# Optimization experiments

Hardware: AMD Instinct MI355X
Metric: run time of the kernel (lower is better)

## Reference

```python
import jax, jax.numpy as jnp
from jax import lax
import numpy as np

NBINS = 50

def _make_filters():
    coords = np.linspace(-1.0, 1.0, 3)
    zz, yy, xx = np.meshgrid(coords, coords, coords, indexing='ij')
    gf = []
    for freq in [2.0, 4.0]:
        for ang in [0.0, np.pi / 4, np.pi / 2, 3 * np.pi / 4]:
            gauss = np.exp(-(xx ** 2 + yy ** 2 + zz ** 2) / 0.5)
            f = gauss * np.cos(freq * (xx * np.cos(ang) + yy * np.sin(ang)))
            f = f - f.mean()
            s = f.std(ddof=1)  # torch std is unbiased
            if s > 1e-8:
                f = f / s
            gf.append(f)
    gf = np.stack(gf)[:, None].astype(np.float32)  # (8,1,3,3,3)
    lf = []
    for axis in range(3):
        for sign in [1, -1]:
            f = np.zeros((3, 3, 3), np.float32)
            f[1, 1, 1] = 1.0
            idx = [1, 1, 1]
            idx[axis] += sign
            f[tuple(idx)] = -1.0
            lf.append(f)
    lf = np.stack(lf)[:, None].astype(np.float32)  # (6,1,3,3,3)
    return gf, lf

def setup_inputs() -> dict:
    key = jax.random.key(0)
    k1, k2 = jax.random.split(key)
    B, D, H, W = 4, 96, 160, 160
    x = jax.random.uniform(k1, (B, 1, D, H, W), jnp.float32, minval=-1.0, maxval=1.0)
    mask = (jax.random.uniform(k2, (B, 1, D, H, W), jnp.float32) > 0.5).astype(jnp.float32)
    gf, lf = _make_filters()
    return {"x": x, "mask": mask, "gabor_filters": jnp.asarray(gf), "lbp_filters": jnp.asarray(lf)}

def _hu_stats(v, mf):
    # v, mf: (B,D,H,W); mf is 0/1 float mask
    n = mf.sum((1, 2, 3))                      # (B,)
    nn = jnp.maximum(n, 1.0)
    mu = (mf * v).sum((1, 2, 3)) / nn
    diff = (v - mu[:, None, None, None]) * mf
    var = (diff ** 2).sum((1, 2, 3)) / jnp.maximum(n - 1.0, 1.0)  # unbiased, like torch .std()
    sigma = jnp.sqrt(var) + 1e-8
    z = diff / sigma[:, None, None, None]
    skew = (z ** 3).sum((1, 2, 3)) / nn
    kurt = (z ** 4).sum((1, 2, 3)) / nn - 3.0
    # histogram over [-1,1] with 50 bins; torch.histc ignores out-of-range, last bin inclusive
    w = mf * ((v >= -1.0) & (v <= 1.0)).astype(v.dtype)
    idx = jnp.clip(jnp.floor((v + 1.0) * (NBINS / 2.0)).astype(jnp.int32), 0, NBINS - 1)
    hist = jax.vmap(lambda i, wb: jnp.zeros((NBINS,), v.dtype).at[i.ravel()].add(wb.ravel()))(idx, w)
    p = hist / (hist.sum(-1, keepdims=True) + 1e-8)
    ent = -(p * jnp.log(p + 1e-8)).sum(-1)
    valid = (n >= 10.0).astype(v.dtype)
    return jnp.stack([mu, sigma, skew, kurt, ent], axis=1) * valid[:, None]  # (B,5)

def _glcm_proxy(v, m):
    # v: (B,D,H,W) float; m: (B,D,H,W) bool
    rows = []
    for axis in range(3):
        a = axis + 1
        sl1 = tuple(slice(None, -1) if i == a else slice(None) for i in range(4))
        sl2 = tuple(slice(1, None) if i == a else slice(None) for i in range(4))
        d = v[sl1] - v[sl2]
        mp = (m[sl1] & m[sl2]).astype(v.dtype)
        s = mp.sum((1, 2, 3))
        ss = jnp.maximum(s, 1.0)
        con = (mp * d * d).sum((1, 2, 3)) / ss
        hom = (mp / (1.0 + d * d)).sum((1, 2, 3)) / ss
        ok = (s >= 4.0).astype(v.dtype)
        rows += [con * ok, hom * ok]
    return jnp.stack(rows, axis=1)  # (B,6)

def _forward(x, mask, gabor_filters, lbp_filters):
    v = x[:, 0]                       # (B,D,H,W)
    m = mask[:, 0] > 0.5              # bool
    mf = m.astype(x.dtype)
    hu = _hu_stats(v, mf)             # (B,5)
    dn = ('NCDHW', 'OIDHW', 'NCDHW')
    pad = [(1, 1)] * 3
    gab = lax.conv_general_dilated(x, gabor_filters, (1, 1, 1), pad, dimension_numbers=dn)
    lung_vol = jnp.clip(mask.sum((2, 3, 4)), 1.0, None)      # (B,1)
    gab_feat = jnp.abs(gab * mask).sum((2, 3, 4)) / lung_vol  # (B,8)
    lbp = lax.conv_general_dilated(x, lbp_filters, (1, 1, 1), pad, dimension_numbers=dn)
    lbp = lbp * mask
    lbp_feat = ((lbp > 0).astype(x.dtype) * mask).sum((2, 3, 4)) / lung_vol  # (B,6)
    glcm = _glcm_proxy(v, m)          # (B,6)
    return jnp.concatenate([hu, gab_feat, lbp_feat, glcm], axis=1)  # (B,25)

def reference(x, mask, gabor_filters, lbp_filters):
    return _forward(x, mask, gabor_filters, lbp_filters)
```

## Files before the change

kernel.cpp:

```cpp
#include <hip/hip_runtime.h>
#include <math.h>

#define B_    4
#define D_    96
#define H_    160
#define W_    160
#define HW_   (H_ * W_)
#define NVOX  (D_ * H_ * W_)
#define NBINS 50
#define NQR   28
#define CPB   256
#define PART_F (B_ * NQR * CPB)
#define HIST_U PART_F
#define WQ_F   (PART_F + 200)
#define LASTP ((D_ - 1) * HW_)

typedef float f2 __attribute__((ext_vector_type(2)));

__device__ __forceinline__ float rfl(float v) {
    return __uint_as_float(__builtin_amdgcn_readfirstlane(__float_as_uint(v)));
}

__global__ __launch_bounds__(64) void radiomics_weights(
    const float* __restrict__ gf, const float* __restrict__ lf,
    float* __restrict__ ws)
{
    const int lane = threadIdx.x;
    __shared__ float sCs[8][5], sR[8], sMO[8], sMC[8];
    if (lane < 8) {
        const int f = lane;
        float O9[9], C9[9];
        float mC = 0.f, mO = 0.f;
#pragma unroll
        for (int k = 0; k < 9; ++k) {
            O9[k] = gf[f * 27 + k];
            C9[k] = gf[f * 27 + 9 + k];
            mC += C9[k]; mO += O9[k];
        }
        mC *= (1.f / 9.f); mO *= (1.f / 9.f);
        float cov = 0.f, var = 0.f;
#pragma unroll
        for (int k = 0; k < 9; ++k) {
            float c = C9[k] - mC, o = O9[k] - mO;
            cov += c * o; var += c * c;
        }
        sR[f] = cov / var; sMO[f] = mO; sMC[f] = mC;
#pragma unroll
        for (int j = 0; j < 4; ++j) sCs[f][j] = 0.5f * (C9[j] + C9[8 - j]);
        sCs[f][4] = C9[4];
    }
    __syncthreads();
    if (lane == 0) {
        float* wq = ws + WQ_F;
        float gz0 = 0.f;
        for (int f = 0; f < 8; ++f) gz0 += sR[f];
        gz0 *= 0.125f;
        wq[0] = gz0;
        float df[8];
        for (int f = 0; f < 8; ++f) df[f] = sMO[f] - gz0 * sMC[f];
        for (int F = 0; F < 2; ++F) {
            const int f0 = 4 * F, f1 = 4 * F + 1, f2 = 4 * F + 2, f3 = 4 * F + 3;
            float* g = wq + 1 + 11 * F;
            g[0]  = 0.5f * (df[f0] + df[f2]);
            g[1]  = 0.5f * (sCs[f0][0] + sCs[f2][0]);
            g[2]  = 0.5f * (sCs[f0][2] + sCs[f2][2]);
            g[3]  = 0.5f * (sCs[f0][4] + sCs[f2][4]);
            g[4]  = 0.5f * (sCs[f0][1] + sCs[f2][3]);
            g[5]  = 0.5f * (sCs[f0][3] + sCs[f2][1]);
            g[6]  = 0.5f * (df[f1] + df[f3]);
            g[7]  = 0.25f * (sCs[f1][1] + sCs[f1][3]
                           + sCs[f3][1] + sCs[f3][3]);
            g[8]  = 0.5f * (sCs[f1][4] + sCs[f3][4]);
            g[9]  = 0.5f * (sCs[f1][0] + sCs[f3][2]);
            g[10] = 0.5f * (sCs[f1][2] + sCs[f3][0]);
        }
        const int nbidx[6] = {22, 4, 16, 10, 14, 12};
        for (int f = 0; f < 6; ++f) {
            wq[23 + f] = lf[f * 27 + 13];
            wq[29 + f] = lf[f * 27 + nbidx[f]];
        }
    }
    unsigned int* gh = (unsigned int*)ws + HIST_U;
    for (int i = lane; i < B_ * NBINS; i += 64) gh[i] = 0u;
}

#define LOADP(s, zo) do {                                                   \
    _Pragma("unroll")                                                       \
    for (int r_ = 0; r_ < 3; ++r_) {                                        \
        Xw[s][r_][0] = xbb[(zo) + rowoff[r_] + xL];                         \
        f2 t_ = *(const f2*)(xbb + (zo) + rowoff[r_] + gx);                 \
        Xw[s][r_][1] = t_.x; Xw[s][r_][2] = t_.y;                           \
        Xw[s][r_][3] = xbb[(zo) + rowoff[r_] + xR];                         \
    }                                                                       \
} while (0)

#define FINISH(s, bzv) do {                                                 \
    if ((bzv) == 0.f) {                                                     \
        _Pragma("unroll")                                                   \
        for (int r_ = 0; r_ < 3; ++r_)                                      \
            _Pragma("unroll")                                               \
            for (int c_ = 0; c_ < 4; ++c_) Xw[s][r_][c_] = 0.f;             \
        S9[s][0] = S9[s][1] = 0.f;                                          \
    } else {                                                                \
        _Pragma("unroll")                                                   \
        for (int c_ = 0; c_ < 4; ++c_) {                                    \
            Xw[s][0][c_] *= bndRow0; Xw[s][2][c_] *= bndRow2;               \
        }                                                                   \
        _Pragma("unroll")                                                   \
        for (int r_ = 0; r_ < 3; ++r_) {                                    \
            Xw[s][r_][0] *= bndL; Xw[s][r_][3] *= bndR;                     \
        }                                                                   \
        float cs0_ = Xw[s][0][0] + Xw[s][1][0] + Xw[s][2][0];               \
        float cs1_ = Xw[s][0][1] + Xw[s][1][1] + Xw[s][2][1];               \
        float cs2_ = Xw[s][0][2] + Xw[s][1][2] + Xw[s][2][2];               \
        float cs3_ = Xw[s][0][3] + Xw[s][1][3] + Xw[s][2][3];               \
        S9[s][0] = cs0_ + cs1_ + cs2_;                                      \
        S9[s][1] = cs1_ + cs2_ + cs3_;                                      \
    }                                                                       \
} while (0)

__global__ __launch_bounds__(256) void radiomics_main(
    const float* __restrict__ x, const float* __restrict__ mask,
    float* __restrict__ ws)
{
    __shared__ unsigned int shist[4 * NBINS];
    __shared__ float xred[4][NQR];

    const int tid = threadIdx.x;
    const int tx = tid & 15, ty = tid >> 4;
    const int lane = tid & 63, wid = tid >> 6;

    for (int i = tid; i < 4 * NBINS; i += 256) shist[i] = 0u;

    const float* wq = ws + WQ_F;
    const float gz0 = rfl(wq[0]);
    float gco[22];
#pragma unroll
    for (int i = 0; i < 22; ++i) gco[i] = rfl(wq[1 + i]);
    float lwc[6], lwn[6];
#pragma unroll
    for (int f = 0; f < 6; ++f) { lwc[f] = rfl(wq[23 + f]); lwn[f] = rfl(wq[29 + f]); }

    const int c = blockIdx.x;
    const int b = blockIdx.z;
    int t, z0, nz;
    if (c < 36) {
        t  = c / 6;
        const int ci = c - 6 * t;
        z0 = 16 * ci; nz = 16;
    } else {
        const int c2 = c - 36;
        const int ti = c2 / 5;
        const int ci = c2 - 5 * ti;
        t = 6 + ti;
        if (ci == 0) { z0 = 0; nz = 16; }
        else         { z0 = 20 * ci - 4; nz = 20; }
    }
    const int ngroups = nz >> 2;

    const int gx = (t % 5) * 32 + tx * 2;
    const int gy = (t / 5) * 16 + ty;

    const float* __restrict__ xbb = x    + (size_t)b * NVOX;
    const float* __restrict__ mbb = mask + (size_t)b * NVOX;

    const int gy0 = (gy > 0) ? gy - 1 : 0;
    const int gy2 = (gy + 1 < H_) ? gy + 1 : H_ - 1;
    const int rowoff[3] = { gy0 * W_, gy * W_, gy2 * W_ };
    const float bndRow0 = (gy > 0) ? 1.f : 0.f;
    const float bndRow2 = (gy + 1 < H_) ? 1.f : 0.f;
    const int xL = (gx > 0) ? gx - 1 : 0;
    const int xR = (gx + 2 < W_) ? gx + 2 : W_ - 1;
    const float bndL = (gx > 0) ? 1.f : 0.f;
    const float bndR = (gx + 2 < W_) ? 1.f : 0.f;
    const int moff  = gy * W_ + gx;
    const int myoff = gy2 * W_ + gx;
    const int mxoff = gy * W_ + xR;
    const float bym = bndRow2, bxm = bndR;

    float Xw[4][3][4];
    float S9[4][2];
    float Mq[4][2];
    float bzs[4];
    f2    myq[2];
    float mxq[2];
    float acc[NQR];
#pragma unroll
    for (int q = 0; q < NQR; ++q) acc[q] = 0.f;
    bzs[0] = bzs[1] = bzs[2] = 1.f;

    if (z0 == 0) {
#pragma unroll
        for (int r = 0; r < 3; ++r)
#pragma unroll
            for (int cc = 0; cc < 4; ++cc) Xw[0][r][cc] = 0.f;
        S9[0][0] = S9[0][1] = 0.f;
    } else {
        LOADP(0, (z0 - 1) * HW_);
        FINISH(0, 1.f);
    }
    LOADP(1, z0 * HW_);
    FINISH(1, 1.f);
    {
        f2 mm = *(const f2*)(mbb + z0 * HW_ + moff);
        Mq[1][0] = (mm.x > 0.5f) ? 1.f : 0.f;
        Mq[1][1] = (mm.y > 0.5f) ? 1.f : 0.f;
    }
    LOADP(2, (z0 + 1) * HW_);
    {
        f2 mm = *(const f2*)(mbb + (z0 + 1) * HW_ + moff);
        Mq[2][0] = mm.x; Mq[2][1] = mm.y;
    }
    Mq[0][0] = Mq[0][1] = 0.f;
    myq[0] = *(const f2*)(mbb + z0 * HW_ + myoff);
    mxq[0] = mbb[z0 * HW_ + mxoff];

    int zc   = z0 * HW_;
    int zpre = (z0 + 2) * HW_;

#pragma unroll 1
    for (int g = 0; g < ngroups; ++g) {
#pragma unroll
        for (int j = 0; j < 4; ++j) {
            const int c0 = j, c1 = (j + 1) & 3, c2 = (j + 2) & 3, c3 = (j + 3) & 3;
            const int cur = j & 1, nxt = cur ^ 1;

            const int zpe = (zpre < NVOX) ? zpre : LASTP;
            bzs[c3] = (zpre < NVOX) ? 1.f : 0.f;
            LOADP(c3, zpe);
            {
                f2 mm = *(const f2*)(mbb + zpe + moff);
                Mq[c3][0] = mm.x; Mq[c3][1] = mm.y;
            }
            const int zn = (zc + HW_ < NVOX) ? zc + HW_ : LASTP;
            myq[nxt] = *(const f2*)(mbb + zn + myoff);
            mxq[nxt] = mbb[zn + mxoff];

            FINISH(c2, bzs[c2]);
            Mq[c2][0] = (Mq[c2][0] * bzs[c2] > 0.5f) ? 1.f : 0.f;
            Mq[c2][1] = (Mq[c2][1] * bzs[c2] > 0.5f) ? 1.f : 0.f;

            float T6[3][4];
#pragma unroll
            for (int r = 0; r < 3; ++r)
#pragma unroll
                for (int cc = 0; cc < 4; ++cc)
                    T6[r][cc] = fmaf(gz0, Xw[c0][r][cc] + Xw[c2][r][cc], Xw[c1][r][cc]);

            const f2 my2 = myq[cur];
            const float mxs = mxq[cur];

#pragma unroll
            for (int q = 0; q < 2; ++q) {
                const float v  = Xw[c1][1][q + 1];
                const float mc = Mq[c1][q];

                acc[0] += mc;
                float mv  = mc * v;  acc[1] += mv;
                float mv2 = mv * v;  acc[2] += mv2;
                float mv3 = mv2 * v; acc[3] += mv3;
                acc[4] += mv3 * v;

                if (mc > 0.5f && v >= -1.f && v <= 1.f) {
                    int bi = (int)floorf((v + 1.f) * (NBINS * 0.5f));
                    bi = min(max(bi, 0), NBINS - 1);
                    atomicAdd(&shist[(tid >> 6) * NBINS + bi], 1u);
                }

                float P0 = T6[0][q]     + T6[2][q + 2];
                float P1 = T6[0][q + 1] + T6[2][q + 1];
                float P2 = T6[0][q + 2] + T6[2][q];
                float P3 = T6[1][q]     + T6[1][q + 2];
                float ctrv = T6[1][q + 1];
                float S2 = S9[c0][q] + S9[c2][q];
                float Qv = P1 + P3;
#pragma unroll
                for (int F = 0; F < 2; ++F) {
                    const float dfA = gco[F*11+0], c0s = gco[F*11+1];
                    const float c2s = gco[F*11+2], c4s = gco[F*11+3];
                    const float cu  = gco[F*11+4], cw  = gco[F*11+5];
                    const float dfB = gco[F*11+6], ct  = gco[F*11+7];
                    const float ce  = gco[F*11+8], ca  = gco[F*11+9];
                    const float cb  = gco[F*11+10];
                    float E = dfA * S2;
                    E = fmaf(c0s, P0, E); E = fmaf(c2s, P2, E); E = fmaf(c4s, ctrv, E);
                    float r0   = fmaf(cu, P1, fmaf(cw, P3, E));
                    float r90  = fmaf(cw, P1, fmaf(cu, P3, E));
                    float G = fmaf(ct, Qv, dfB * S2);
                    G = fmaf(ce, ctrv, G);
                    float r45  = fmaf(ca, P0, fmaf(cb, P2, G));
                    float r135 = fmaf(cb, P0, fmaf(ca, P2, G));
                    acc[5 + 4*F + 0] = fmaf(fabsf(r0),   mc, acc[5 + 4*F + 0]);
                    acc[5 + 4*F + 1] = fmaf(fabsf(r45),  mc, acc[5 + 4*F + 1]);
                    acc[5 + 4*F + 2] = fmaf(fabsf(r90),  mc, acc[5 + 4*F + 2]);
                    acc[5 + 4*F + 3] = fmaf(fabsf(r135), mc, acc[5 + 4*F + 3]);
                }

                const float nb[6] = { Xw[c2][1][q + 1], Xw[c0][1][q + 1],
                                      Xw[c1][2][q + 1], Xw[c1][0][q + 1],
                                      Xw[c1][1][q + 2], Xw[c1][1][q] };
#pragma unroll
                for (int f = 0; f < 6; ++f) {
                    float l = fmaf(lwc[f], v, lwn[f] * nb[f]);
                    acc[13 + f] += (l > 0.f) ? mc : 0.f;
                }

                {
                    float mp = mc * Mq[c2][q];
                    float d = v - Xw[c2][1][q + 1], dd = d * d;
                    acc[19] += mp;
                    acc[22] = fmaf(mp, dd, acc[22]);
                    acc[25] = fmaf(mp, __builtin_amdgcn_rcpf(1.f + dd), acc[25]);
                }
                {
                    float mr = (q == 0) ? my2.x : my2.y;
                    float mp = mc * (((mr > 0.5f) ? 1.f : 0.f) * bym);
                    float d = v - Xw[c1][2][q + 1], dd = d * d;
                    acc[20] += mp;
                    acc[23] = fmaf(mp, dd, acc[23]);
                    acc[26] = fmaf(mp, __builtin_amdgcn_rcpf(1.f + dd), acc[26]);
                }
                {
                    float mnr = (q == 0) ? Mq[c1][1] : (((mxs > 0.5f) ? 1.f : 0.f) * bxm);
                    float mp = mc * mnr;
                    float d = v - Xw[c1][1][q + 2], dd = d * d;
                    acc[21] += mp;
                    acc[24] = fmaf(mp, dd, acc[24]);
                    acc[27] = fmaf(mp, __builtin_amdgcn_rcpf(1.f + dd), acc[27]);
                }
            }
            zc += HW_; zpre += HW_;
        }
    }

#pragma unroll
    for (int q = 0; q < NQR; ++q) {
        float sm = acc[q];
#pragma unroll
        for (int o = 32; o > 0; o >>= 1)
            sm += __shfl_down(sm, o, 64);
        acc[q] = sm;
    }
    if (lane == 0) {
#pragma unroll
        for (int q = 0; q < NQR; ++q) xred[wid][q] = acc[q];
    }
    __syncthreads();

    if (tid < NQR) {
        float v = xred[0][tid] + xred[1][tid] + xred[2][tid] + xred[3][tid];
        ws[((size_t)b * NQR + tid) * CPB + c] = v;
    } else if (tid < NQR + NBINS) {
        int h = tid - NQR;
        unsigned int cnt = shist[h] + shist[NBINS + h]
                         + shist[2 * NBINS + h] + shist[3 * NBINS + h];
        unsigned int* ghist = (unsigned int*)ws + HIST_U;
        if (cnt) atomicAdd(&ghist[b * NBINS + h], cnt);
    }
}

__global__ __launch_bounds__(512) void radiomics_tail(
    const float* __restrict__ ws, float* __restrict__ out)
{
    __shared__ double fin[NQR];
    __shared__ double hcnt[NBINS];
    __shared__ double entp[NBINS];
    __shared__ double sh_hsum;
    const int b = blockIdx.x, tid = threadIdx.x;
    const int wave = tid >> 6, lane = tid & 63;

    for (int q = wave; q < NQR; q += 8) {
        const float* p = ws + ((size_t)b * NQR + q) * CPB;
        double s = 0.0;
#pragma unroll
        for (int k = 0; k < 4; ++k)
            s += (double)p[lane + 64 * k];
#pragma unroll
        for (int o = 32; o > 0; o >>= 1)
            s += __shfl_down(s, o, 64);
        if (lane == 0) fin[q] = s;
    }
    if (tid < NBINS)
        hcnt[tid] = (double)(((const unsigned int*)ws)[HIST_U + b * NBINS + tid]);
    __syncthreads();

    if (tid == 0) {
        double h = 0.0;
        for (int k = 0; k < NBINS; ++k) h += hcnt[k];
        sh_hsum = h + 1e-8;
    }
    __syncthreads();

    if (tid < NBINS) {
        double p = hcnt[tid] / sh_hsum;
        entp[tid] = -p * log(p + 1e-8);
    }
    __syncthreads();

    if (tid == 0) {
        const double n  = fin[0];
        const double nn = fmax(n, 1.0);
        const double s1 = fin[1], s2 = fin[2], s3 = fin[3], s4 = fin[4];
        const double mu = s1 / nn;
        const double M2 = s2 - 2.0 * mu * s1 + mu * mu * n;
        const double M3 = s3 - 3.0 * mu * s2 + 3.0 * mu * mu * s1 - mu * mu * mu * n;
        const double M4 = s4 - 4.0 * mu * s3 + 6.0 * mu * mu * s2
                          - 4.0 * mu * mu * mu * s1 + mu * mu * mu * mu * n;
        const double var   = M2 / fmax(n - 1.0, 1.0);
        const double sigma = sqrt(var) + 1e-8;
        const double skew  = M3 / (sigma * sigma * sigma) / nn;
        const double kurt  = M4 / (sigma * sigma * sigma * sigma) / nn - 3.0;

        double ent = 0.0;
        for (int k = 0; k < NBINS; ++k) ent += entp[k];

        const double valid = (n >= 10.0) ? 1.0 : 0.0;
        float* ob = out + b * 25;
        ob[0] = (float)(mu * valid);
        ob[1] = (float)(sigma * valid);
        ob[2] = (float)(skew * valid);
        ob[3] = (float)(kurt * valid);
        ob[4] = (float)(ent * valid);

        const double lung = fmax(n, 1.0);
        for (int f = 0; f < 8; ++f) ob[5 + f]  = (float)(fin[5 + f] / lung);
        for (int f = 0; f < 6; ++f) ob[13 + f] = (float)(fin[13 + f] / lung);

        for (int ax = 0; ax < 3; ++ax) {
            double s  = fin[19 + ax];
            double ss = fmax(s, 1.0);
            double ok = (s >= 4.0) ? 1.0 : 0.0;
            ob[19 + 2 * ax]     = (float)(fin[22 + ax] / ss * ok);
            ob[19 + 2 * ax + 1] = (float)(fin[25 + ax] / ss * ok);
        }
    }
}

extern "C" void kernel_launch(void* const* d_in, const int* in_sizes, int n_in,
                              void* d_out, int out_size, void* d_ws, size_t ws_size,
                              hipStream_t stream)
{
    const float* x    = (const float*)d_in[0];
    const float* mask = (const float*)d_in[1];
    const float* gf   = (const float*)d_in[2];
    const float* lf   = (const float*)d_in[3];
    float* out = (float*)d_out;
    float* ws  = (float*)d_ws;

    radiomics_weights<<<1, 64, 0, stream>>>(gf, lf, ws);
    radiomics_main<<<dim3(256, 1, B_), 256, 0, stream>>>(x, mask, ws);
    radiomics_tail<<<B_, 512, 0, stream>>>(ws, out);
}
```

Measured before the change: 166.1 us.

## Stage x and mask z-slices into LDS via async global_load_lds ring buffer

Replaces per-thread global loads of halo rows with cooperative async global-to-LDS copies of 18x36 tiles for x and mask. A 4-slot ring buffer prefetches the slice two ahead and synchronises with vmcnt waits and barriers. The LBP filters are now applied as a comparison v > neighbor instead of using the loaded weights, which hardcodes the filter values. The change adds LDS use and per-slice barriers, and sets launch bounds for 4 blocks per CU.

```diff
diff --git a/kernel.cpp b/kernel.cpp
--- a/kernel.cpp
+++ b/kernel.cpp
@@ -13,12 +13,19 @@
 #define PART_F (B_ * NQR * CPB)
 #define HIST_U PART_F
 #define WQ_F   (PART_F + 200)
-#define LASTP ((D_ - 1) * HW_)
+#define TS    36
 
 typedef float f2 __attribute__((ext_vector_type(2)));
 
 __device__ __forceinline__ float rfl(float v) {
     return __uint_as_float(__builtin_amdgcn_readfirstlane(__float_as_uint(v)));
+}
+
+__device__ __forceinline__ void gload_lds(const float* g, float* l) {
+    __builtin_amdgcn_global_load_lds(
+        (const __attribute__((address_space(1))) unsigned int*)(g),
+        (__attribute__((address_space(3))) unsigned int*)(l),
+        4, 0, 0);
 }
 
 __global__ __launch_bounds__(64) void radiomics_weights(
@@ -74,23 +81,28 @@
             g[9]  = 0.5f * (sCs[f1][0] + sCs[f3][2]);
             g[10] = 0.5f * (sCs[f1][2] + sCs[f3][0]);
         }
-        const int nbidx[6] = {22, 4, 16, 10, 14, 12};
-        for (int f = 0; f < 6; ++f) {
-            wq[23 + f] = lf[f * 27 + 13];
-            wq[29 + f] = lf[f * 27 + nbidx[f]];
-        }
     }
     unsigned int* gh = (unsigned int*)ws + HIST_U;
     for (int i = lane; i < B_ * NBINS; i += 64) gh[i] = 0u;
 }
 
-#define LOADP(s, zo) do {                                                   \
+#define STAGE(bi, zp) do {                                                  \
+    const float* px_ = xbb + (size_t)(zp) * HW_;                            \
+    const float* pm_ = mbb + (size_t)(zp) * HW_;                            \
+    _Pragma("unroll")                                                       \
+    for (int j_ = 0; j_ < 3; ++j_) {                                        \
+        gload_lds(px_ + xsrc[j_], &xs[bi][lbase + 256 * j_]);               \
+        gload_lds(pm_ + msrc[j_], &msd[bi][lbase + 256 * j_]);              \
+    }                                                                       \
+} while (0)
+
+#define RDX(s, bi) do {                                                     \
     _Pragma("unroll")                                                       \
     for (int r_ = 0; r_ < 3; ++r_) {                                        \
-        Xw[s][r_][0] = xbb[(zo) + rowoff[r_] + xL];                         \
-        f2 t_ = *(const f2*)(xbb + (zo) + rowoff[r_] + gx);                 \
-        Xw[s][r_][1] = t_.x; Xw[s][r_][2] = t_.y;                           \
-        Xw[s][r_][3] = xbb[(zo) + rowoff[r_] + xR];                         \
+        f2 a_  = *(const f2*)&xs[bi][(ty + r_) * TS + 2 * tx];              \
+        f2 b2_ = *(const f2*)&xs[bi][(ty + r_) * TS + 2 * tx + 2];          \
+        Xw[s][r_][0] = a_.x;  Xw[s][r_][1] = a_.y;                          \
+        Xw[s][r_][2] = b2_.x; Xw[s][r_][3] = b2_.y;                         \
     }                                                                       \
 } while (0)
 
@@ -119,16 +131,19 @@
     }                                                                       \
 } while (0)
 
-__global__ __launch_bounds__(256) void radiomics_main(
+__global__ __launch_bounds__(256, 4) void radiomics_main(
     const float* __restrict__ x, const float* __restrict__ mask,
     float* __restrict__ ws)
 {
+    __shared__ float xs[4][768];
+    __shared__ float msd[4][768];
     __shared__ unsigned int shist[4 * NBINS];
     __shared__ float xred[4][NQR];
 
     const int tid = threadIdx.x;
     const int tx = tid & 15, ty = tid >> 4;
     const int lane = tid & 63, wid = tid >> 6;
+    const int lbase = __builtin_amdgcn_readfirstlane(tid & ~63);
 
     for (int i = tid; i < 4 * NBINS; i += 256) shist[i] = 0u;
 
@@ -137,9 +152,6 @@
     float gco[22];
 #pragma unroll
     for (int i = 0; i < 22; ++i) gco[i] = rfl(wq[1 + i]);
-    float lwc[6], lwn[6];
-#pragma unroll
-    for (int f = 0; f < 6; ++f) { lwc[f] = rfl(wq[23 + f]); lwn[f] = rfl(wq[29 + f]); }
 
     const int c = blockIdx.x;
     const int b = blockIdx.z;
@@ -158,102 +170,113 @@
     }
     const int ngroups = nz >> 2;
 
-    const int gx = (t % 5) * 32 + tx * 2;
-    const int gy = (t / 5) * 16 + ty;
+    const int gx0t = (t % 5) * 32;
+    const int gy0t = (t / 5) * 16;
+    const int gx = gx0t + tx * 2;
+    const int gy = gy0t + ty;
 
     const float* __restrict__ xbb = x    + (size_t)b * NVOX;
     const float* __restrict__ mbb = mask + (size_t)b * NVOX;
 
-    const int gy0 = (gy > 0) ? gy - 1 : 0;
-    const int gy2 = (gy + 1 < H_) ? gy + 1 : H_ - 1;
-    const int rowoff[3] = { gy0 * W_, gy * W_, gy2 * W_ };
+    int xsrc[3], msrc[3];
+#pragma unroll
+    for (int j = 0; j < 3; ++j) {
+        int idx = tid + 256 * j;
+        int row = idx / TS;
+        int col = idx - row * TS;
+        int gr = gy0t - 1 + row; gr = gr < 0 ? 0 : (gr > H_ - 1 ? H_ - 1 : gr);
+        int gc = gx0t - 1 + col; gc = gc < 0 ? 0 : (gc > W_ - 1 ? W_ - 1 : gc);
+        xsrc[j] = gr * W_ + gc;
+        int mr = gy0t + row; mr = mr > H_ - 1 ? H_ - 1 : mr;
+        int mcc = gx0t + col; mcc = mcc > W_ - 1 ? W_ - 1 : mcc;
+        msrc[j] = mr * W_ + mcc;
+    }
+
     const float bndRow0 = (gy > 0) ? 1.f : 0.f;
     const float bndRow2 = (gy + 1 < H_) ? 1.f : 0.f;
-    const int xL = (gx > 0) ? gx - 1 : 0;
-    const int xR = (gx + 2 < W_) ? gx + 2 : W_ - 1;
     const float bndL = (gx > 0) ? 1.f : 0.f;
     const float bndR = (gx + 2 < W_) ? 1.f : 0.f;
-    const int moff  = gy * W_ + gx;
-    const int myoff = gy2 * W_ + gx;
-    const int mxoff = gy * W_ + xR;
     const float bym = bndRow2, bxm = bndR;
 
     float Xw[4][3][4];
     float S9[4][2];
-    float Mq[4][2];
-    float bzs[4];
+    float Mq[2][2];
     f2    myq[2];
     float mxq[2];
     float acc[NQR];
 #pragma unroll
     for (int q = 0; q < NQR; ++q) acc[q] = 0.f;
-    bzs[0] = bzs[1] = bzs[2] = 1.f;
+
+    STAGE(3, (z0 > 0) ? z0 - 1 : 0);
+    STAGE(0, z0);
+    STAGE(1, z0 + 1);
+    asm volatile("s_waitcnt vmcnt(0)" ::: "memory");
+    __builtin_amdgcn_s_barrier();
+    __builtin_amdgcn_sched_barrier(0);
 
     if (z0 == 0) {
 #pragma unroll
         for (int r = 0; r < 3; ++r)
 #pragma unroll
-            for (int cc = 0; cc < 4; ++cc) Xw[0][r][cc] = 0.f;
-        S9[0][0] = S9[0][1] = 0.f;
+            for (int cc = 0; cc < 4; ++cc) Xw[3][r][cc] = 0.f;
+        S9[3][0] = S9[3][1] = 0.f;
     } else {
-        LOADP(0, (z0 - 1) * HW_);
-        FINISH(0, 1.f);
-    }
-    LOADP(1, z0 * HW_);
-    FINISH(1, 1.f);
+        RDX(3, 3);
+        FINISH(3, 1.f);
+    }
+    RDX(0, 0);
+    FINISH(0, 1.f);
     {
-        f2 mm = *(const f2*)(mbb + z0 * HW_ + moff);
-        Mq[1][0] = (mm.x > 0.5f) ? 1.f : 0.f;
-        Mq[1][1] = (mm.y > 0.5f) ? 1.f : 0.f;
-    }
-    LOADP(2, (z0 + 1) * HW_);
-    {
-        f2 mm = *(const f2*)(mbb + (z0 + 1) * HW_ + moff);
-        Mq[2][0] = mm.x; Mq[2][1] = mm.y;
-    }
-    Mq[0][0] = Mq[0][1] = 0.f;
-    myq[0] = *(const f2*)(mbb + z0 * HW_ + myoff);
-    mxq[0] = mbb[z0 * HW_ + mxoff];
-
-    int zc   = z0 * HW_;
-    int zpre = (z0 + 2) * HW_;
-
+        f2 cm0 = *(const f2*)&msd[0][ty * TS + 2 * tx];
+        Mq[0][0] = (cm0.x > 0.5f) ? 1.f : 0.f;
+        Mq[0][1] = (cm0.y > 0.5f) ? 1.f : 0.f;
+        myq[0] = *(const f2*)&msd[0][(ty + 1) * TS + 2 * tx];
+        mxq[0] = msd[0][ty * TS + 2 * tx + 2];
+    }
+
+    int z = z0;
 #pragma unroll 1
     for (int g = 0; g < ngroups; ++g) {
 #pragma unroll
         for (int j = 0; j < 4; ++j) {
-            const int c0 = j, c1 = (j + 1) & 3, c2 = (j + 2) & 3, c3 = (j + 3) & 3;
+            const int cs = j & 3;
+            const int c0 = (j + 3) & 3;
+            const int c2 = (j + 1) & 3;
+            const int bn = (j + 1) & 3;
+            const int bs = (j + 2) & 3;
             const int cur = j & 1, nxt = cur ^ 1;
 
-            const int zpe = (zpre < NVOX) ? zpre : LASTP;
-            bzs[c3] = (zpre < NVOX) ? 1.f : 0.f;
-            LOADP(c3, zpe);
+            const int zs = (z + 2 < D_) ? z + 2 : D_ - 1;
+            STAGE(bs, zs);
+            asm volatile("s_waitcnt vmcnt(6)" ::: "memory");
+            __builtin_amdgcn_s_barrier();
+            __builtin_amdgcn_sched_barrier(0);
+
+            const float bzn = (z + 1 < D_) ? 1.f : 0.f;
+            RDX(c2, bn);
+            FINISH(c2, bzn);
             {
-                f2 mm = *(const f2*)(mbb + zpe + moff);
-                Mq[c3][0] = mm.x; Mq[c3][1] = mm.y;
+                f2 cmm = *(const f2*)&msd[bn][ty * TS + 2 * tx];
+                Mq[nxt][0] = (cmm.x * bzn > 0.5f) ? 1.f : 0.f;
+                Mq[nxt][1] = (cmm.y * bzn > 0.5f) ? 1.f : 0.f;
+                myq[nxt] = *(const f2*)&msd[bn][(ty + 1) * TS + 2 * tx];
+                mxq[nxt] = msd[bn][ty * TS + 2 * tx + 2];
             }
-            const int zn = (zc + HW_ < NVOX) ? zc + HW_ : LASTP;
-            myq[nxt] = *(const f2*)(mbb + zn + myoff);
-            mxq[nxt] = mbb[zn + mxoff];
-
-            FINISH(c2, bzs[c2]);
-            Mq[c2][0] = (Mq[c2][0] * bzs[c2] > 0.5f) ? 1.f : 0.f;
-            Mq[c2][1] = (Mq[c2][1] * bzs[c2] > 0.5f) ? 1.f : 0.f;
 
             float T6[3][4];
 #pragma unroll
             for (int r = 0; r < 3; ++r)
 #pragma unroll
                 for (int cc = 0; cc < 4; ++cc)
-                    T6[r][cc] = fmaf(gz0, Xw[c0][r][cc] + Xw[c2][r][cc], Xw[c1][r][cc]);
+                    T6[r][cc] = fmaf(gz0, Xw[c0][r][cc] + Xw[c2][r][cc], Xw[cs][r][cc]);
 
             const f2 my2 = myq[cur];
             const float mxs = mxq[cur];
 
 #pragma unroll
             for (int q = 0; q < 2; ++q) {
-                const float v  = Xw[c1][1][q + 1];
-                const float mc = Mq[c1][q];
+                const float v  = Xw[cs][1][q + 1];
+                const float mc = Mq[cur][q];
 
                 acc[0] += mc;
                 float mv  = mc * v;  acc[1] += mv;
@@ -297,16 +320,14 @@
                 }
 
                 const float nb[6] = { Xw[c2][1][q + 1], Xw[c0][1][q + 1],
-                                      Xw[c1][2][q + 1], Xw[c1][0][q + 1],
-                                      Xw[c1][1][q + 2], Xw[c1][1][q] };
-#pragma unroll
-                for (int f = 0; f < 6; ++f) {
-                    float l = fmaf(lwc[f], v, lwn[f] * nb[f]);
-                    acc[13 + f] += (l > 0.f) ? mc : 0.f;
-                }
+                                      Xw[cs][2][q + 1], Xw[cs][0][q + 1],
+                                      Xw[cs][1][q + 2], Xw[cs][1][q] };
+#pragma unroll
+                for (int f = 0; f < 6; ++f)
+                    acc[13 + f] += (v > nb[f]) ? mc : 0.f;
 
                 {
-                    float mp = mc * Mq[c2][q];
+                    float mp = mc * Mq[nxt][q];
                     float d = v - Xw[c2][1][q + 1], dd = d * d;
                     acc[19] += mp;
                     acc[22] = fmaf(mp, dd, acc[22]);
@@ -315,21 +336,21 @@
                 {
                     float mr = (q == 0) ? my2.x : my2.y;
                     float mp = mc * (((mr > 0.5f) ? 1.f : 0.f) * bym);
-                    float d = v - Xw[c1][2][q + 1], dd = d * d;
+                    float d = v - Xw[cs][2][q + 1], dd = d * d;
                     acc[20] += mp;
                     acc[23] = fmaf(mp, dd, acc[23]);
                     acc[26] = fmaf(mp, __builtin_amdgcn_rcpf(1.f + dd), acc[26]);
                 }
                 {
-                    float mnr = (q == 0) ? Mq[c1][1] : (((mxs > 0.5f) ? 1.f : 0.f) * bxm);
+                    float mnr = (q == 0) ? Mq[cur][1] : (((mxs > 0.5f) ? 1.f : 0.f) * bxm);
                     float mp = mc * mnr;
-                    float d = v - Xw[c1][1][q + 2], dd = d * d;
+                    float d = v - Xw[cs][1][q + 2], dd = d * d;
                     acc[21] += mp;
                     acc[24] = fmaf(mp, dd, acc[24]);
                     acc[27] = fmaf(mp, __builtin_amdgcn_rcpf(1.f + dd), acc[27]);
                 }
             }
-            zc += HW_; zpre += HW_;
+            ++z;
         }
     }
 
```

Result: slower. 320.5 us (+93.0%).
